# Kernel optimization log

Measured on AMD Instinct MI355X. Metric: run time of the kernel, lower is better.

## Reference

```python
import jax, jax.numpy as jnp
import numpy as np

MUL = 32          # channel multiplicity
N_NODES = 50000
N_EDGES = 800000
IN_DIM = 4 * MUL      # 32x0e + 32x1o (ir_mul layout: 1o block is (3, MUL))
SH_DIM = 4            # 0e + 1o
W_DIM = 5 * MUL       # 5 CG paths, per-channel weights
OUT_DIM = 7 * MUL     # 32x0e + 32x1o + 32x1e
INV_SQRT3 = 0.5773502691896258
INV_SQRT2 = 0.7071067811865476


def setup_inputs() -> dict:
    key = jax.random.key(0)
    k1, k2, k3, k4 = jax.random.split(key, 4)
    node_features = jax.random.normal(k1, (N_NODES, IN_DIM), dtype=jnp.float32)
    edge_angular = jax.random.normal(k2, (N_EDGES, SH_DIM), dtype=jnp.float32)
    edge_index = jax.random.randint(k3, (N_EDGES, 2), 0, N_NODES, dtype=jnp.int64)
    tp_weights = jax.random.normal(k4, (N_EDGES, W_DIM), dtype=jnp.float32)
    return {"node_features": node_features, "edge_angular": edge_angular,
            "edge_index": edge_index, "tp_weights": tp_weights}


def reference(node_features, edge_angular, edge_index, tp_weights):
    n_nodes = node_features.shape[0]
    src = edge_index[:, 0]
    dst = edge_index[:, 1]

    # gather sender node features per edge
    h = node_features[src]                       # (E, 4*MUL)
    h0 = h[:, :MUL]                              # (E, MUL)       32x0e
    h1 = h[:, MUL:].reshape(-1, 3, MUL)          # (E, 3, MUL)    32x1o, ir_mul layout

    y0 = edge_angular[:, 0:1]                    # (E, 1)   0e
    y1 = edge_angular[:, 1:4]                    # (E, 3)   1o

    w = tp_weights.reshape(-1, 5, MUL)           # (E, 5, MUL) per-path per-channel

    # path 0: 0e (x) 0e -> 0e ; path 3: 1o (x) 1o -> 0e (dot / sqrt(3))
    dot = jnp.einsum('emc,em->ec', h1, y1)       # (E, MUL)
    out0e = w[:, 0] * h0 * y0 + w[:, 3] * (INV_SQRT3 * dot)

    # path 1: 0e (x) 1o -> 1o ; path 2: 1o (x) 0e -> 1o
    out1o = (w[:, 1][:, None, :] * h0[:, None, :] * y1[:, :, None]
             + w[:, 2][:, None, :] * h1 * y0[:, :, None])     # (E, 3, MUL)

    # path 4: 1o (x) 1o -> 1e (cross / sqrt(2))
    c0 = h1[:, 1] * y1[:, 2, None] - h1[:, 2] * y1[:, 1, None]
    c1 = h1[:, 2] * y1[:, 0, None] - h1[:, 0] * y1[:, 2, None]
    c2 = h1[:, 0] * y1[:, 1, None] - h1[:, 1] * y1[:, 0, None]
    cross = jnp.stack([c0, c1, c2], axis=1)                   # (E, 3, MUL)
    out1e = w[:, 4][:, None, :] * (INV_SQRT2 * cross)

    msg = jnp.concatenate([out0e,
                           out1o.reshape(-1, 3 * MUL),
                           out1e.reshape(-1, 3 * MUL)], axis=1)  # (E, 7*MUL)

    # scatter-add messages into receiver nodes (size_out = n_nodes)
    out = jax.ops.segment_sum(msg, dst, num_segments=n_nodes)    # (N, 7*MUL)
    return out
```

## Files before the change

kernel.cpp:

```cpp
#include <hip/hip_runtime.h>


#define IN_DIM 128
#define W_DIM 160
#define OUT_DIM 224

typedef float vf4 __attribute__((ext_vector_type(4)));

__device__ __forceinline__ float elem(const float4& v, int i) {
    return ((const float*)&v)[i];
}

__global__ void __launch_bounds__(256) hist_dst(
    const int2* __restrict__ eidx2, int* __restrict__ counts, int n_edges)
{
    int e = blockIdx.x * blockDim.x + threadIdx.x;
    if (e >= n_edges) return;
    atomicAdd(counts + eidx2[e].y, 1);
}

__global__ void __launch_bounds__(256) block_sums(
    const int* __restrict__ counts, int* __restrict__ bsums, int n)
{
    int idx = blockIdx.x * 256 + threadIdx.x;
    int x = (idx < n) ? counts[idx] : 0;
    #pragma unroll
    for (int off = 1; off < 64; off <<= 1) x += __shfl_xor(x, off);
    __shared__ int ws[4];
    if ((threadIdx.x & 63) == 0) ws[threadIdx.x >> 6] = x;
    __syncthreads();
    if (threadIdx.x == 0) bsums[blockIdx.x] = ws[0] + ws[1] + ws[2] + ws[3];
}

__global__ void __launch_bounds__(256) scan_block_sums(
    int* __restrict__ bsums, int* __restrict__ total_out, int nb)
{
    __shared__ int wsum[4];
    __shared__ int carry_s;
    int tid = threadIdx.x;
    int lane = tid & 63, wid = tid >> 6;
    if (tid == 0) carry_s = 0;
    __syncthreads();

    for (int base = 0; base < nb; base += 256) {
        int idx = base + tid;
        int x = (idx < nb) ? bsums[idx] : 0;
        int incl = x;
        #pragma unroll
        for (int off = 1; off < 64; off <<= 1) {
            int v = __shfl_up(incl, off);
            if (lane >= off) incl += v;
        }
        if (lane == 63) wsum[wid] = incl;
        __syncthreads();
        int wpre = 0;
        #pragma unroll
        for (int k = 0; k < 4; ++k) if (k < wid) wpre += wsum[k];
        int carry = carry_s;
        int excl = incl - x + wpre + carry;
        if (idx < nb) bsums[idx] = excl;
        __syncthreads();
        if (tid == 255) carry_s = carry + wpre + incl;
        __syncthreads();
    }
    if (tid == 0) *total_out = carry_s;
}

__global__ void __launch_bounds__(256) scan_final(
    int* __restrict__ counts, int* __restrict__ cursor,
    const int* __restrict__ bsums, int n)
{
    int idx = blockIdx.x * 256 + threadIdx.x;
    int x = (idx < n) ? counts[idx] : 0;
    int lane = threadIdx.x & 63, wid = threadIdx.x >> 6;
    int incl = x;
    #pragma unroll
    for (int off = 1; off < 64; off <<= 1) {
        int v = __shfl_up(incl, off);
        if (lane >= off) incl += v;
    }
    __shared__ int wsum[4];
    if (lane == 63) wsum[wid] = incl;
    __syncthreads();
    int wpre = 0;
    #pragma unroll
    for (int k = 0; k < 4; ++k) if (k < wid) wpre += wsum[k];
    int excl = incl - x + wpre + bsums[blockIdx.x];
    if (idx < n) {
        counts[idx] = excl;
        cursor[idx] = excl;
    }
}

__global__ void __launch_bounds__(256) scatter_edges(
    const int2* __restrict__ eidx2, int* __restrict__ cursor,
    int2* __restrict__ pairs, int n_edges)
{
    int e = blockIdx.x * blockDim.x + threadIdx.x;
    if (e >= n_edges) return;
    int2 sd = eidx2[e];
    int pos = atomicAdd(cursor + sd.y, 1);
    pairs[pos] = make_int2(e, sd.x);
}

__global__ void __launch_bounds__(256) gather_nodes(
    const float* __restrict__ nf,
    const float* __restrict__ ang,
    const float* __restrict__ w,
    const int*  __restrict__ offsets,
    const int2* __restrict__ pairs,
    float* __restrict__ out,
    int n_nodes)
{
    const float INV_SQRT3 = 0.5773502691896258f;
    const float INV_SQRT2 = 0.7071067811865476f;

    int gtid = blockIdx.x * blockDim.x + threadIdx.x;
    int node = gtid >> 6;
    if (node >= n_nodes) return;
    int lane = threadIdx.x & 63;
    int c    = lane & 31;
    int half = lane >> 5;

    int start = offsets[node];
    int end   = offsets[node + 1];

    float a0 = 0.f, a1 = 0.f, a2 = 0.f, a3 = 0.f, a4 = 0.f, a5 = 0.f, a6 = 0.f;

    auto body = [&](int2 p) {
        int e = p.x, s = p.y;
        vf4 y = __builtin_nontemporal_load((const vf4*)(ang + 4 * (size_t)e));
        const float* hp = nf + (size_t)s * IN_DIM + c;
        float h0 = hp[0];
        float ha = hp[32];
        float hb = hp[64];
        float hc = hp[96];
        const float* wp = w + (size_t)e * W_DIM + c;
        float w0 = __builtin_nontemporal_load(wp);
        float w1 = __builtin_nontemporal_load(wp + 32);
        float w2 = __builtin_nontemporal_load(wp + 64);
        float w3 = __builtin_nontemporal_load(wp + 96);
        float w4 = __builtin_nontemporal_load(wp + 128);

        float dot = ha * y[1] + hb * y[2] + hc * y[3];
        a0 += w0 * h0 * y[0] + w3 * (INV_SQRT3 * dot);
        a1 += w1 * h0 * y[1] + w2 * ha * y[0];
        a2 += w1 * h0 * y[2] + w2 * hb * y[0];
        a3 += w1 * h0 * y[3] + w2 * hc * y[0];
        float w4s = w4 * INV_SQRT2;
        a4 += w4s * (hb * y[3] - hc * y[2]);
        a5 += w4s * (hc * y[1] - ha * y[3]);
        a6 += w4s * (ha * y[2] - hb * y[1]);
    };

    int i = start + half;
    for (; i + 2 < end; i += 4) {
        int2 pa = pairs[i];
        int2 pb = pairs[i + 2];
        body(pa);
        body(pb);
    }
    if (i < end) body(pairs[i]);

    a0 += __shfl_xor(a0, 32);
    a1 += __shfl_xor(a1, 32);
    a2 += __shfl_xor(a2, 32);
    a3 += __shfl_xor(a3, 32);
    a4 += __shfl_xor(a4, 32);
    a5 += __shfl_xor(a5, 32);
    a6 += __shfl_xor(a6, 32);

    if (half == 0) {
        float* op = out + (size_t)node * OUT_DIM + c;
        __builtin_nontemporal_store(a0, op);
        __builtin_nontemporal_store(a1, op + 32);
        __builtin_nontemporal_store(a2, op + 64);
        __builtin_nontemporal_store(a3, op + 96);
        __builtin_nontemporal_store(a4, op + 128);
        __builtin_nontemporal_store(a5, op + 160);
        __builtin_nontemporal_store(a6, op + 192);
    }
}

__global__ void __launch_bounds__(256) conv_tp_edges_atomic(
    const float* __restrict__ nf,
    const float* __restrict__ ang,
    const int*   __restrict__ eidx,
    const float* __restrict__ w,
    float* __restrict__ out,
    int n_edges)
{
    const float INV_SQRT3 = 0.5773502691896258f;
    const float INV_SQRT2 = 0.7071067811865476f;

    int tid = blockIdx.x * blockDim.x + threadIdx.x;
    int e = tid >> 3;
    int t = tid & 7;
    if (e >= n_edges) return;

    int src = eidx[2 * e];
    int dst = eidx[2 * e + 1];
    float4 y = *(const float4*)(ang + 4 * (size_t)e);

    const float* hp = nf + (size_t)src * IN_DIM + 4 * t;
    float4 h0  = *(const float4*)(hp);
    float4 h1a = *(const float4*)(hp + 32);
    float4 h1b = *(const float4*)(hp + 64);
    float4 h1c = *(const float4*)(hp + 96);

    const float* wp = w + (size_t)e * W_DIM + 4 * t;
    float4 w0 = *(const float4*)(wp);
    float4 w1 = *(const float4*)(wp + 32);
    float4 w2 = *(const float4*)(wp + 64);
    float4 w3 = *(const float4*)(wp + 96);
    float4 w4 = *(const float4*)(wp + 128);

    float* op = out + (size_t)dst * OUT_DIM + 4 * t;

    #pragma unroll
    for (int i = 0; i < 4; ++i) {
        float h0c = elem(h0, i), ha = elem(h1a, i), hb = elem(h1b, i), hc = elem(h1c, i);
        float dot = ha * y.y + hb * y.z + hc * y.w;
        atomicAdd(op + i, elem(w0, i) * h0c * y.x + elem(w3, i) * (INV_SQRT3 * dot));
        float w1c = elem(w1, i), w2c = elem(w2, i);
        atomicAdd(op + 32 + i, w1c * h0c * y.y + w2c * ha * y.x);
        atomicAdd(op + 64 + i, w1c * h0c * y.z + w2c * hb * y.x);
        atomicAdd(op + 96 + i, w1c * h0c * y.w + w2c * hc * y.x);
        float w4c = elem(w4, i) * INV_SQRT2;
        atomicAdd(op + 128 + i, w4c * (hb * y.w - hc * y.z));
        atomicAdd(op + 160 + i, w4c * (hc * y.y - ha * y.w));
        atomicAdd(op + 192 + i, w4c * (ha * y.z - hb * y.y));
    }
}

extern "C" void kernel_launch(void* const* d_in, const int* in_sizes, int n_in,
                              void* d_out, int out_size, void* d_ws, size_t ws_size,
                              hipStream_t stream) {
    const float* nf   = (const float*)d_in[0];
    const float* ang  = (const float*)d_in[1];
    const int*   eidx = (const int*)d_in[2];
    const float* w    = (const float*)d_in[3];
    float* out = (float*)d_out;

    int n_edges = in_sizes[2] / 2;
    int n_nodes = out_size / OUT_DIM;
    int nb = (n_nodes + 255) / 256;

    size_t off_counts = 0;
    size_t off_cursor = off_counts + (size_t)(n_nodes + 1);
    size_t off_bsums  = off_cursor + (size_t)n_nodes;
    size_t off_pairs  = (off_bsums + (size_t)nb + 1) & ~(size_t)1;
    size_t ints_needed = off_pairs + 2 * (size_t)n_edges;
    size_t bytes_needed = ints_needed * sizeof(int);

    if (ws_size < bytes_needed) {
        hipMemsetAsync(d_out, 0, (size_t)out_size * sizeof(float), stream);
        int threads_total = n_edges * 8;
        int grid = (threads_total + 255) / 256;
        conv_tp_edges_atomic<<<grid, 256, 0, stream>>>(nf, ang, eidx, w, out, n_edges);
        return;
    }

    int* counts  = (int*)d_ws + off_counts;
    int* cursor  = (int*)d_ws + off_cursor;
    int* bsums   = (int*)d_ws + off_bsums;
    int2* pairs  = (int2*)((int*)d_ws + off_pairs);

    hipMemsetAsync(counts, 0, (size_t)(n_nodes + 1) * sizeof(int), stream);

    int grid_e = (n_edges + 255) / 256;
    hist_dst<<<grid_e, 256, 0, stream>>>((const int2*)eidx, counts, n_edges);
    block_sums<<<nb, 256, 0, stream>>>(counts, bsums, n_nodes);
    scan_block_sums<<<1, 256, 0, stream>>>(bsums, counts + n_nodes, nb);
    scan_final<<<nb, 256, 0, stream>>>(counts, cursor, bsums, n_nodes);
    scatter_edges<<<grid_e, 256, 0, stream>>>((const int2*)eidx, cursor, pairs, n_edges);

    int threads_total = n_nodes * 64;
    int grid_g = (threads_total + 255) / 256;
    gather_nodes<<<grid_g, 256, 0, stream>>>(nf, ang, w, counts, pairs, out, n_nodes);
}
```

Measured before the change: 806.8 us.

## Software-pipeline gather loop with contiguous halves and two edges per thread in CSR build

```diff
diff --git a/kernel.cpp b/kernel.cpp
--- a/kernel.cpp
+++ b/kernel.cpp
@@ -6,17 +6,25 @@
 #define OUT_DIM 224
 
 typedef float vf4 __attribute__((ext_vector_type(4)));
+typedef int   vi4 __attribute__((ext_vector_type(4), aligned(8)));
 
 __device__ __forceinline__ float elem(const float4& v, int i) {
     return ((const float*)&v)[i];
 }
 
 __global__ void __launch_bounds__(256) hist_dst(
-    const int2* __restrict__ eidx2, int* __restrict__ counts, int n_edges)
-{
-    int e = blockIdx.x * blockDim.x + threadIdx.x;
-    if (e >= n_edges) return;
-    atomicAdd(counts + eidx2[e].y, 1);
+    const int* __restrict__ eidx, int* __restrict__ counts, int n_edges)
+{
+    int t = blockIdx.x * blockDim.x + threadIdx.x;
+    int e0 = 2 * t;
+    if (e0 >= n_edges) return;
+    if (e0 + 1 < n_edges) {
+        int4 q = *(const int4*)(eidx + 4 * (size_t)t);
+        atomicAdd(counts + q.y, 1);
+        atomicAdd(counts + q.w, 1);
+    } else {
+        atomicAdd(counts + eidx[2 * e0 + 1], 1);
+    }
 }
 
 __global__ void __launch_bounds__(256) block_sums(
@@ -93,15 +101,31 @@
 }
 
 __global__ void __launch_bounds__(256) scatter_edges(
-    const int2* __restrict__ eidx2, int* __restrict__ cursor,
+    const int* __restrict__ eidx, int* __restrict__ cursor,
     int2* __restrict__ pairs, int n_edges)
 {
-    int e = blockIdx.x * blockDim.x + threadIdx.x;
-    if (e >= n_edges) return;
-    int2 sd = eidx2[e];
-    int pos = atomicAdd(cursor + sd.y, 1);
-    pairs[pos] = make_int2(e, sd.x);
-}
+    int t = blockIdx.x * blockDim.x + threadIdx.x;
+    int e0 = 2 * t;
+    if (e0 >= n_edges) return;
+    if (e0 + 1 < n_edges) {
+        int4 q = *(const int4*)(eidx + 4 * (size_t)t);
+        int pos0 = atomicAdd(cursor + q.y, 1);
+        pairs[pos0] = make_int2(e0, q.x);
+        int pos1 = atomicAdd(cursor + q.w, 1);
+        pairs[pos1] = make_int2(e0 + 1, q.z);
+    } else {
+        int src = eidx[2 * e0];
+        int dst = eidx[2 * e0 + 1];
+        int pos = atomicAdd(cursor + dst, 1);
+        pairs[pos] = make_int2(e0, src);
+    }
+}
+
+struct EdgeRegs {
+    vf4  y;
+    float h0, ha, hb, hc;
+    float w0, w1, w2, w3, w4;
+};
 
 __global__ void __launch_bounds__(256) gather_nodes(
     const float* __restrict__ nf,
@@ -124,43 +148,72 @@
 
     int start = offsets[node];
     int end   = offsets[node + 1];
-
-    float a0 = 0.f, a1 = 0.f, a2 = 0.f, a3 = 0.f, a4 = 0.f, a5 = 0.f, a6 = 0.f;
-
-    auto body = [&](int2 p) {
-        int e = p.x, s = p.y;
-        vf4 y = __builtin_nontemporal_load((const vf4*)(ang + 4 * (size_t)e));
+    int cnt   = end - start;
+    int mid   = start + ((cnt + 1) >> 1);
+    int lo    = half ? mid : start;
+    int hi    = half ? end : mid;
+
+    auto load_edge = [&](EdgeRegs& E, int e, int s) {
+        const float* wp = w + (size_t)e * W_DIM + c;
+        E.w0 = __builtin_nontemporal_load(wp);
+        E.w1 = __builtin_nontemporal_load(wp + 32);
+        E.w2 = __builtin_nontemporal_load(wp + 64);
+        E.w3 = __builtin_nontemporal_load(wp + 96);
+        E.w4 = __builtin_nontemporal_load(wp + 128);
+        E.y  = __builtin_nontemporal_load((const vf4*)(ang + 4 * (size_t)e));
         const float* hp = nf + (size_t)s * IN_DIM + c;
-        float h0 = hp[0];
-        float ha = hp[32];
-        float hb = hp[64];
-        float hc = hp[96];
-        const float* wp = w + (size_t)e * W_DIM + c;
-        float w0 = __builtin_nontemporal_load(wp);
-        float w1 = __builtin_nontemporal_load(wp + 32);
-        float w2 = __builtin_nontemporal_load(wp + 64);
-        float w3 = __builtin_nontemporal_load(wp + 96);
-        float w4 = __builtin_nontemporal_load(wp + 128);
-
-        float dot = ha * y[1] + hb * y[2] + hc * y[3];
-        a0 += w0 * h0 * y[0] + w3 * (INV_SQRT3 * dot);
-        a1 += w1 * h0 * y[1] + w2 * ha * y[0];
-        a2 += w1 * h0 * y[2] + w2 * hb * y[0];
-        a3 += w1 * h0 * y[3] + w2 * hc * y[0];
-        float w4s = w4 * INV_SQRT2;
-        a4 += w4s * (hb * y[3] - hc * y[2]);
-        a5 += w4s * (hc * y[1] - ha * y[3]);
-        a6 += w4s * (ha * y[2] - hb * y[1]);
+        E.h0 = hp[0];
+        E.ha = hp[32];
+        E.hb = hp[64];
+        E.hc = hp[96];
     };
 
-    int i = start + half;
-    for (; i + 2 < end; i += 4) {
-        int2 pa = pairs[i];
-        int2 pb = pairs[i + 2];
-        body(pa);
-        body(pb);
-    }
-    if (i < end) body(pairs[i]);
+    float aA0 = 0.f, aA1 = 0.f, aA2 = 0.f, aA3 = 0.f, aA4 = 0.f, aA5 = 0.f, aA6 = 0.f;
+    float aB0 = 0.f, aB1 = 0.f, aB2 = 0.f, aB3 = 0.f, aB4 = 0.f, aB5 = 0.f, aB6 = 0.f;
+
+    #define COMPUTE(E, s0, s1, s2, s3, s4, s5, s6)                           \
+        do {                                                                 \
+            float dot = E.ha * E.y[1] + E.hb * E.y[2] + E.hc * E.y[3];       \
+            s0 += E.w0 * E.h0 * E.y[0] + E.w3 * (INV_SQRT3 * dot);           \
+            s1 += E.w1 * E.h0 * E.y[1] + E.w2 * E.ha * E.y[0];               \
+            s2 += E.w1 * E.h0 * E.y[2] + E.w2 * E.hb * E.y[0];               \
+            s3 += E.w1 * E.h0 * E.y[3] + E.w2 * E.hc * E.y[0];               \
+            float w4s = E.w4 * INV_SQRT2;                                    \
+            s4 += w4s * (E.hb * E.y[3] - E.hc * E.y[2]);                     \
+            s5 += w4s * (E.hc * E.y[1] - E.ha * E.y[3]);                     \
+            s6 += w4s * (E.ha * E.y[2] - E.hb * E.y[1]);                     \
+        } while (0)
+
+    int i = lo;
+    if (i + 1 < hi) {
+        vi4 q = *(const vi4*)(pairs + i);
+        EdgeRegs E0, E1;
+        load_edge(E0, q.x, q.y);
+        load_edge(E1, q.z, q.w);
+        i += 2;
+        for (; i + 1 < hi; i += 2) {
+            vi4 qn = *(const vi4*)(pairs + i);
+            EdgeRegs N0, N1;
+            load_edge(N0, qn.x, qn.y);
+            load_edge(N1, qn.z, qn.w);
+            COMPUTE(E0, aA0, aA1, aA2, aA3, aA4, aA5, aA6);
+            COMPUTE(E1, aB0, aB1, aB2, aB3, aB4, aB5, aB6);
+            E0 = N0;
+            E1 = N1;
+        }
+        COMPUTE(E0, aA0, aA1, aA2, aA3, aA4, aA5, aA6);
+        COMPUTE(E1, aB0, aB1, aB2, aB3, aB4, aB5, aB6);
+    }
+    if (i < hi) {
+        int2 p = pairs[i];
+        EdgeRegs E;
+        load_edge(E, p.x, p.y);
+        COMPUTE(E, aA0, aA1, aA2, aA3, aA4, aA5, aA6);
+    }
+    #undef COMPUTE
+
+    float a0 = aA0 + aB0, a1 = aA1 + aB1, a2 = aA2 + aB2, a3 = aA3 + aB3;
+    float a4 = aA4 + aB4, a5 = aA5 + aB5, a6 = aA6 + aB6;
 
     a0 += __shfl_xor(a0, 32);
     a1 += __shfl_xor(a1, 32);
@@ -268,12 +321,13 @@
 
     hipMemsetAsync(counts, 0, (size_t)(n_nodes + 1) * sizeof(int), stream);
 
-    int grid_e = (n_edges + 255) / 256;
-    hist_dst<<<grid_e, 256, 0, stream>>>((const int2*)eidx, counts, n_edges);
+    int half_e = (n_edges + 1) / 2;
+    int grid_e2 = (half_e + 255) / 256;
+    hist_dst<<<grid_e2, 256, 0, stream>>>(eidx, counts, n_edges);
     block_sums<<<nb, 256, 0, stream>>>(counts, bsums, n_nodes);
     scan_block_sums<<<1, 256, 0, stream>>>(bsums, counts + n_nodes, nb);
     scan_final<<<nb, 256, 0, stream>>>(counts, cursor, bsums, n_nodes);
-    scatter_edges<<<grid_e, 256, 0, stream>>>((const int2*)eidx, cursor, pairs, n_edges);
+    scatter_edges<<<grid_e2, 256, 0, stream>>>(eidx, cursor, pairs, n_edges);
 
     int threads_total = n_nodes * 64;
     int grid_g = (threads_total + 255) / 256;
```

After: 796.6 us. No clear change (-1.3%).

## Replace CSR scan with fixed-capacity per-node buckets in one cooperative fused kernel

Applied to the files above, without the earlier changes.

```diff
diff --git a/kernel.cpp b/kernel.cpp
--- a/kernel.cpp
+++ b/kernel.cpp
@@ -1,198 +1,215 @@
 #include <hip/hip_runtime.h>
+#include <hip/hip_cooperative_groups.h>
+
+namespace cg = cooperative_groups;
 
 
 #define IN_DIM 128
 #define W_DIM 160
 #define OUT_DIM 224
+#define SPILL_CAP 4096
 
 typedef float vf4 __attribute__((ext_vector_type(4)));
+
+#define INV_SQRT3f 0.5773502691896258f
+#define INV_SQRT2f 0.7071067811865476f
+
+
+__device__ __forceinline__ void scatter_phase(
+    const int* __restrict__ eidx, int* __restrict__ cursor,
+    int* __restrict__ spill_cnt, int4* __restrict__ spill,
+    int2* __restrict__ buckets, int cap, int n_edges, int tid, int nthreads)
+{
+    int n_half = (n_edges + 1) >> 1;
+    for (int t = tid; t < n_half; t += nthreads) {
+        int e0 = 2 * t;
+        if (e0 + 1 < n_edges) {
+            int4 q = *(const int4*)(eidx + 4 * (size_t)t);
+            int p0 = atomicAdd(cursor + q.y, 1);
+            if (p0 < cap) buckets[(size_t)q.y * cap + p0] = make_int2(e0, q.x);
+            else { int sp = atomicAdd(spill_cnt, 1); if (sp < SPILL_CAP) spill[sp] = make_int4(e0, q.x, q.y, 0); }
+            int p1 = atomicAdd(cursor + q.w, 1);
+            if (p1 < cap) buckets[(size_t)q.w * cap + p1] = make_int2(e0 + 1, q.z);
+            else { int sp = atomicAdd(spill_cnt, 1); if (sp < SPILL_CAP) spill[sp] = make_int4(e0 + 1, q.z, q.w, 0); }
+        } else {
+            int src = eidx[2 * e0];
+            int dst = eidx[2 * e0 + 1];
+            int p = atomicAdd(cursor + dst, 1);
+            if (p < cap) buckets[(size_t)dst * cap + p] = make_int2(e0, src);
+            else { int sp = atomicAdd(spill_cnt, 1); if (sp < SPILL_CAP) spill[sp] = make_int4(e0, src, dst, 0); }
+        }
+    }
+}
+
+__device__ __forceinline__ void gather_phase(
+    const float* __restrict__ nf, const float* __restrict__ ang,
+    const float* __restrict__ w, const int* __restrict__ cursor,
+    const int2* __restrict__ buckets, int cap, float* __restrict__ out,
+    int n_nodes, int wave_id, int n_waves, int lane)
+{
+    int c    = lane & 31;
+    int half = lane >> 5;
+
+    for (int node = wave_id; node < n_nodes; node += n_waves) {
+        int cnt = cursor[node];
+        if (cnt > cap) cnt = cap;
+        const int2* bp = buckets + (size_t)node * cap;
+        int mid = (cnt + 1) >> 1;
+        int lo = half ? mid : 0;
+        int hi = half ? cnt : mid;
+
+        float a0 = 0.f, a1 = 0.f, a2 = 0.f, a3 = 0.f, a4 = 0.f, a5 = 0.f, a6 = 0.f;
+
+        for (int i = lo; i < hi; ++i) {
+            int2 p = bp[i];
+            int e = p.x, s = p.y;
+            vf4 y = __builtin_nontemporal_load((const vf4*)(ang + 4 * (size_t)e));
+            const float* hp = nf + (size_t)s * IN_DIM + c;
+            float h0 = hp[0];
+            float ha = hp[32];
+            float hb = hp[64];
+            float hc = hp[96];
+            const float* wp = w + (size_t)e * W_DIM + c;
+            float w0 = __builtin_nontemporal_load(wp);
+            float w1 = __builtin_nontemporal_load(wp + 32);
+            float w2 = __builtin_nontemporal_load(wp + 64);
+            float w3 = __builtin_nontemporal_load(wp + 96);
+            float w4 = __builtin_nontemporal_load(wp + 128);
+
+            float dot = ha * y[1] + hb * y[2] + hc * y[3];
+            a0 += w0 * h0 * y[0] + w3 * (INV_SQRT3f * dot);
+            a1 += w1 * h0 * y[1] + w2 * ha * y[0];
+            a2 += w1 * h0 * y[2] + w2 * hb * y[0];
+            a3 += w1 * h0 * y[3] + w2 * hc * y[0];
+            float w4s = w4 * INV_SQRT2f;
+            a4 += w4s * (hb * y[3] - hc * y[2]);
+            a5 += w4s * (hc * y[1] - ha * y[3]);
+            a6 += w4s * (ha * y[2] - hb * y[1]);
+        }
+
+        a0 += __shfl_xor(a0, 32);
+        a1 += __shfl_xor(a1, 32);
+        a2 += __shfl_xor(a2, 32);
+        a3 += __shfl_xor(a3, 32);
+        a4 += __shfl_xor(a4, 32);
+        a5 += __shfl_xor(a5, 32);
+        a6 += __shfl_xor(a6, 32);
+
+        if (half == 0) {
+            float* op = out + (size_t)node * OUT_DIM + c;
+            __builtin_nontemporal_store(a0, op);
+            __builtin_nontemporal_store(a1, op + 32);
+            __builtin_nontemporal_store(a2, op + 64);
+            __builtin_nontemporal_store(a3, op + 96);
+            __builtin_nontemporal_store(a4, op + 128);
+            __builtin_nontemporal_store(a5, op + 160);
+            __builtin_nontemporal_store(a6, op + 192);
+        }
+    }
+}
+
+__device__ __forceinline__ void spill_phase(
+    const float* __restrict__ nf, const float* __restrict__ ang,
+    const float* __restrict__ w, const int4* __restrict__ spill,
+    int n_spill, float* __restrict__ out, int tid, int nthreads)
+{
+    for (int i = tid; i < n_spill; i += nthreads) {
+        int4 s4 = spill[i];
+        int e = s4.x, s = s4.y, dst = s4.z;
+        vf4 y = *(const vf4*)(ang + 4 * (size_t)e);
+        for (int c = 0; c < 32; ++c) {
+            float h0 = nf[(size_t)s * IN_DIM + c];
+            float ha = nf[(size_t)s * IN_DIM + 32 + c];
+            float hb = nf[(size_t)s * IN_DIM + 64 + c];
+            float hc = nf[(size_t)s * IN_DIM + 96 + c];
+            const float* wp = w + (size_t)e * W_DIM + c;
+            float w0 = wp[0], w1 = wp[32], w2 = wp[64], w3 = wp[96], w4 = wp[128];
+            float* op = out + (size_t)dst * OUT_DIM + c;
+            float dot = ha * y[1] + hb * y[2] + hc * y[3];
+            atomicAdd(op,       w0 * h0 * y[0] + w3 * (INV_SQRT3f * dot));
+            atomicAdd(op + 32,  w1 * h0 * y[1] + w2 * ha * y[0]);
+            atomicAdd(op + 64,  w1 * h0 * y[2] + w2 * hb * y[0]);
+            atomicAdd(op + 96,  w1 * h0 * y[3] + w2 * hc * y[0]);
+            float w4s = w4 * INV_SQRT2f;
+            atomicAdd(op + 128, w4s * (hb * y[3] - hc * y[2]));
+            atomicAdd(op + 160, w4s * (hc * y[1] - ha * y[3]));
+            atomicAdd(op + 192, w4s * (ha * y[2] - hb * y[1]));
+        }
+    }
+}
+
+
+__global__ void __launch_bounds__(256, 4) fused_conv(
+    const float* __restrict__ nf, const float* __restrict__ ang,
+    const int* __restrict__ eidx, const float* __restrict__ w,
+    int* __restrict__ cursor, int* __restrict__ spill_cnt,
+    int4* __restrict__ spill, int2* __restrict__ buckets,
+    float* __restrict__ out, int n_edges, int n_nodes, int cap)
+{
+    cg::grid_group grid = cg::this_grid();
+    int tid = blockIdx.x * blockDim.x + threadIdx.x;
+    int nthreads = gridDim.x * blockDim.x;
+
+    scatter_phase(eidx, cursor, spill_cnt, spill, buckets, cap, n_edges, tid, nthreads);
+
+    __threadfence();
+    grid.sync();
+
+    int lane = threadIdx.x & 63;
+    int wave_id = tid >> 6;
+    int n_waves = nthreads >> 6;
+    gather_phase(nf, ang, w, cursor, buckets, cap, out, n_nodes, wave_id, n_waves, lane);
+
+    __threadfence();
+    grid.sync();
+
+    int n_spill = *spill_cnt;
+    if (n_spill > SPILL_CAP) n_spill = SPILL_CAP;
+    spill_phase(nf, ang, w, spill, n_spill, out, tid, nthreads);
+}
+
+
+__global__ void __launch_bounds__(256) scatter_k(
+    const int* __restrict__ eidx, int* __restrict__ cursor,
+    int* __restrict__ spill_cnt, int4* __restrict__ spill,
+    int2* __restrict__ buckets, int cap, int n_edges)
+{
+    int tid = blockIdx.x * blockDim.x + threadIdx.x;
+    scatter_phase(eidx, cursor, spill_cnt, spill, buckets, cap, n_edges,
+                  tid, gridDim.x * blockDim.x);
+}
+
+__global__ void __launch_bounds__(256) gather_k(
+    const float* __restrict__ nf, const float* __restrict__ ang,
+    const float* __restrict__ w, const int* __restrict__ cursor,
+    const int2* __restrict__ buckets, int cap, float* __restrict__ out, int n_nodes)
+{
+    int tid = blockIdx.x * blockDim.x + threadIdx.x;
+    gather_phase(nf, ang, w, cursor, buckets, cap, out, n_nodes,
+                 tid >> 6, (gridDim.x * blockDim.x) >> 6, threadIdx.x & 63);
+}
+
+__global__ void __launch_bounds__(256) spill_k(
+    const float* __restrict__ nf, const float* __restrict__ ang,
+    const float* __restrict__ w, const int* __restrict__ spill_cnt,
+    const int4* __restrict__ spill, float* __restrict__ out)
+{
+    int n_spill = *spill_cnt;
+    if (n_spill > SPILL_CAP) n_spill = SPILL_CAP;
+    spill_phase(nf, ang, w, spill, n_spill, out,
+                blockIdx.x * blockDim.x + threadIdx.x, gridDim.x * blockDim.x);
+}
+
 
 __device__ __forceinline__ float elem(const float4& v, int i) {
     return ((const float*)&v)[i];
 }
 
-__global__ void __launch_bounds__(256) hist_dst(
-    const int2* __restrict__ eidx2, int* __restrict__ counts, int n_edges)
-{
-    int e = blockIdx.x * blockDim.x + threadIdx.x;
-    if (e >= n_edges) return;
-    atomicAdd(counts + eidx2[e].y, 1);
-}
-
-__global__ void __launch_bounds__(256) block_sums(
-    const int* __restrict__ counts, int* __restrict__ bsums, int n)
-{
-    int idx = blockIdx.x * 256 + threadIdx.x;
-    int x = (idx < n) ? counts[idx] : 0;
-    #pragma unroll
-    for (int off = 1; off < 64; off <<= 1) x += __shfl_xor(x, off);
-    __shared__ int ws[4];
-    if ((threadIdx.x & 63) == 0) ws[threadIdx.x >> 6] = x;
-    __syncthreads();
-    if (threadIdx.x == 0) bsums[blockIdx.x] = ws[0] + ws[1] + ws[2] + ws[3];
-}
-
-__global__ void __launch_bounds__(256) scan_block_sums(
-    int* __restrict__ bsums, int* __restrict__ total_out, int nb)
-{
-    __shared__ int wsum[4];
-    __shared__ int carry_s;
-    int tid = threadIdx.x;
-    int lane = tid & 63, wid = tid >> 6;
-    if (tid == 0) carry_s = 0;
-    __syncthreads();
-
-    for (int base = 0; base < nb; base += 256) {
-        int idx = base + tid;
-        int x = (idx < nb) ? bsums[idx] : 0;
-        int incl = x;
-        #pragma unroll
-        for (int off = 1; off < 64; off <<= 1) {
-            int v = __shfl_up(incl, off);
-            if (lane >= off) incl += v;
-        }
-        if (lane == 63) wsum[wid] = incl;
-        __syncthreads();
-        int wpre = 0;
-        #pragma unroll
-        for (int k = 0; k < 4; ++k) if (k < wid) wpre += wsum[k];
-        int carry = carry_s;
-        int excl = incl - x + wpre + carry;
-        if (idx < nb) bsums[idx] = excl;
-        __syncthreads();
-        if (tid == 255) carry_s = carry + wpre + incl;
-        __syncthreads();
-    }
-    if (tid == 0) *total_out = carry_s;
-}
-
-__global__ void __launch_bounds__(256) scan_final(
-    int* __restrict__ counts, int* __restrict__ cursor,
-    const int* __restrict__ bsums, int n)
-{
-    int idx = blockIdx.x * 256 + threadIdx.x;
-    int x = (idx < n) ? counts[idx] : 0;
-    int lane = threadIdx.x & 63, wid = threadIdx.x >> 6;
-    int incl = x;
-    #pragma unroll
-    for (int off = 1; off < 64; off <<= 1) {
-        int v = __shfl_up(incl, off);
-        if (lane >= off) incl += v;
-    }
-    __shared__ int wsum[4];
-    if (lane == 63) wsum[wid] = incl;
-    __syncthreads();
-    int wpre = 0;
-    #pragma unroll
-    for (int k = 0; k < 4; ++k) if (k < wid) wpre += wsum[k];
-    int excl = incl - x + wpre + bsums[blockIdx.x];
-    if (idx < n) {
-        counts[idx] = excl;
-        cursor[idx] = excl;
-    }
-}
-
-__global__ void __launch_bounds__(256) scatter_edges(
-    const int2* __restrict__ eidx2, int* __restrict__ cursor,
-    int2* __restrict__ pairs, int n_edges)
-{
-    int e = blockIdx.x * blockDim.x + threadIdx.x;
-    if (e >= n_edges) return;
-    int2 sd = eidx2[e];
-    int pos = atomicAdd(cursor + sd.y, 1);
-    pairs[pos] = make_int2(e, sd.x);
-}
-
-__global__ void __launch_bounds__(256) gather_nodes(
-    const float* __restrict__ nf,
-    const float* __restrict__ ang,
-    const float* __restrict__ w,
-    const int*  __restrict__ offsets,
-    const int2* __restrict__ pairs,
-    float* __restrict__ out,
-    int n_nodes)
-{
-    const float INV_SQRT3 = 0.5773502691896258f;
-    const float INV_SQRT2 = 0.7071067811865476f;
-
-    int gtid = blockIdx.x * blockDim.x + threadIdx.x;
-    int node = gtid >> 6;
-    if (node >= n_nodes) return;
-    int lane = threadIdx.x & 63;
-    int c    = lane & 31;
-    int half = lane >> 5;
-
-    int start = offsets[node];
-    int end   = offsets[node + 1];
-
-    float a0 = 0.f, a1 = 0.f, a2 = 0.f, a3 = 0.f, a4 = 0.f, a5 = 0.f, a6 = 0.f;
-
-    auto body = [&](int2 p) {
-        int e = p.x, s = p.y;
-        vf4 y = __builtin_nontemporal_load((const vf4*)(ang + 4 * (size_t)e));
-        const float* hp = nf + (size_t)s * IN_DIM + c;
-        float h0 = hp[0];
-        float ha = hp[32];
-        float hb = hp[64];
-        float hc = hp[96];
-        const float* wp = w + (size_t)e * W_DIM + c;
-        float w0 = __builtin_nontemporal_load(wp);
-        float w1 = __builtin_nontemporal_load(wp + 32);
-        float w2 = __builtin_nontemporal_load(wp + 64);
-        float w3 = __builtin_nontemporal_load(wp + 96);
-        float w4 = __builtin_nontemporal_load(wp + 128);
-
-        float dot = ha * y[1] + hb * y[2] + hc * y[3];
-        a0 += w0 * h0 * y[0] + w3 * (INV_SQRT3 * dot);
-        a1 += w1 * h0 * y[1] + w2 * ha * y[0];
-        a2 += w1 * h0 * y[2] + w2 * hb * y[0];
-        a3 += w1 * h0 * y[3] + w2 * hc * y[0];
-        float w4s = w4 * INV_SQRT2;
-        a4 += w4s * (hb * y[3] - hc * y[2]);
-        a5 += w4s * (hc * y[1] - ha * y[3]);
-        a6 += w4s * (ha * y[2] - hb * y[1]);
-    };
-
-    int i = start + half;
-    for (; i + 2 < end; i += 4) {
-        int2 pa = pairs[i];
-        int2 pb = pairs[i + 2];
-        body(pa);
-        body(pb);
-    }
-    if (i < end) body(pairs[i]);
-
-    a0 += __shfl_xor(a0, 32);
-    a1 += __shfl_xor(a1, 32);
-    a2 += __shfl_xor(a2, 32);
-    a3 += __shfl_xor(a3, 32);
-    a4 += __shfl_xor(a4, 32);
-    a5 += __shfl_xor(a5, 32);
-    a6 += __shfl_xor(a6, 32);
-
-    if (half == 0) {
-        float* op = out + (size_t)node * OUT_DIM + c;
-        __builtin_nontemporal_store(a0, op);
-        __builtin_nontemporal_store(a1, op + 32);
-        __builtin_nontemporal_store(a2, op + 64);
-        __builtin_nontemporal_store(a3, op + 96);
-        __builtin_nontemporal_store(a4, op + 128);
-        __builtin_nontemporal_store(a5, op + 160);
-        __builtin_nontemporal_store(a6, op + 192);
-    }
-}
-
 __global__ void __launch_bounds__(256) conv_tp_edges_atomic(
-    const float* __restrict__ nf,
-    const float* __restrict__ ang,
-    const int*   __restrict__ eidx,
-    const float* __restrict__ w,
-    float* __restrict__ out,
-    int n_edges)
-{
-    const float INV_SQRT3 = 0.5773502691896258f;
-    const float INV_SQRT2 = 0.7071067811865476f;
-
+    const float* __restrict__ nf, const float* __restrict__ ang,
+    const int* __restrict__ eidx, const float* __restrict__ w,
+    float* __restrict__ out, int n_edges)
+{
     int tid = blockIdx.x * blockDim.x + threadIdx.x;
     int e = tid >> 3;
     int t = tid & 7;
@@ -221,17 +238,18 @@
     for (int i = 0; i < 4; ++i) {
         float h0c = elem(h0, i), ha = elem(h1a, i), hb = elem(h1b, i), hc = elem(h1c, i);
         float dot = ha * y.y + hb * y.z + hc * y.w;
-        atomicAdd(op + i, elem(w0, i) * h0c * y.x + elem(w3, i) * (INV_SQRT3 * dot));
+        atomicAdd(op + i, elem(w0, i) * h0c * y.x + elem(w3, i) * (INV_SQRT3f * dot));
         float w1c = elem(w1, i), w2c = elem(w2, i);
         atomicAdd(op + 32 + i, w1c * h0c * y.y + w2c * ha * y.x);
         atomicAdd(op + 64 + i, w1c * h0c * y.z + w2c * hb * y.x);
         atomicAdd(op + 96 + i, w1c * h0c * y.w + w2c * hc * y.x);
-        float w4c = elem(w4, i) * INV_SQRT2;
+        float w4c = elem(w4, i) * INV_SQRT2f;
         atomicAdd(op + 128 + i, w4c * (hb * y.w - hc * y.z));
         atomicAdd(op + 160 + i, w4c * (hc * y.y - ha * y.w));
         atomicAdd(op + 192 + i, w4c * (ha * y.z - hb * y.y));
     }
 }
+
 
 extern "C" void kernel_launch(void* const* d_in, const int* in_sizes, int n_in,
                               void* d_out, int out_size, void* d_ws, size_t ws_size,
@@ -244,16 +262,18 @@
 
     int n_edges = in_sizes[2] / 2;
     int n_nodes = out_size / OUT_DIM;
-    int nb = (n_nodes + 255) / 256;
-
-    size_t off_counts = 0;
-    size_t off_cursor = off_counts + (size_t)(n_nodes + 1);
-    size_t off_bsums  = off_cursor + (size_t)n_nodes;
-    size_t off_pairs  = (off_bsums + (size_t)nb + 1) & ~(size_t)1;
-    size_t ints_needed = off_pairs + 2 * (size_t)n_edges;
-    size_t bytes_needed = ints_needed * sizeof(int);
-
-    if (ws_size < bytes_needed) {
+
+    size_t off_cursor = 0;
+    size_t off_spillc = off_cursor + (size_t)n_nodes;
+    size_t off_spill  = (off_spillc + 1 + 3) & ~(size_t)3;
+    size_t off_buckets = off_spill + 4 * (size_t)SPILL_CAP;
+
+    int cap = 2048;
+    while (cap >= 64 &&
+           (off_buckets + 2 * (size_t)n_nodes * (size_t)cap) * sizeof(int) > ws_size)
+        cap >>= 1;
+
+    if (cap < 64) {
         hipMemsetAsync(d_out, 0, (size_t)out_size * sizeof(float), stream);
         int threads_total = n_edges * 8;
         int grid = (threads_total + 255) / 256;
@@ -261,21 +281,35 @@
         return;
     }
 
-    int* counts  = (int*)d_ws + off_counts;
-    int* cursor  = (int*)d_ws + off_cursor;
-    int* bsums   = (int*)d_ws + off_bsums;
-    int2* pairs  = (int2*)((int*)d_ws + off_pairs);
-
-    hipMemsetAsync(counts, 0, (size_t)(n_nodes + 1) * sizeof(int), stream);
-
-    int grid_e = (n_edges + 255) / 256;
-    hist_dst<<<grid_e, 256, 0, stream>>>((const int2*)eidx, counts, n_edges);
-    block_sums<<<nb, 256, 0, stream>>>(counts, bsums, n_nodes);
-    scan_block_sums<<<1, 256, 0, stream>>>(bsums, counts + n_nodes, nb);
-    scan_final<<<nb, 256, 0, stream>>>(counts, cursor, bsums, n_nodes);
-    scatter_edges<<<grid_e, 256, 0, stream>>>((const int2*)eidx, cursor, pairs, n_edges);
-
-    int threads_total = n_nodes * 64;
-    int grid_g = (threads_total + 255) / 256;
-    gather_nodes<<<grid_g, 256, 0, stream>>>(nf, ang, w, counts, pairs, out, n_nodes);
-}
+    int*  cursor    = (int*)d_ws + off_cursor;
+    int*  spill_cnt = (int*)d_ws + off_spillc;
+    int4* spill     = (int4*)((int*)d_ws + off_spill);
+    int2* buckets   = (int2*)((int*)d_ws + off_buckets);
+
+    hipMemsetAsync(cursor, 0, ((size_t)n_nodes + 1) * sizeof(int), stream);
+
+    int maxb = 0;
+    hipError_t oe = hipOccupancyMaxActiveBlocksPerMultiprocessor(&maxb, fused_conv, 256, 0);
+    if (oe != hipSuccess || maxb < 1) maxb = 2;
+    if (maxb > 8) maxb = 8;
+    int grid = maxb * 256;
+
+    void* args[] = {
+        (void*)&nf, (void*)&ang, (void*)&eidx, (void*)&w,
+        (void*)&cursor, (void*)&spill_cnt, (void*)&spill, (void*)&buckets,
+        (void*)&out, (void*)&n_edges, (void*)&n_nodes, (void*)&cap
+    };
+    hipError_t le = hipLaunchCooperativeKernel((const void*)fused_conv,
+                                               dim3(grid), dim3(256),
+                                               args, 0, stream);
+    if (le != hipSuccess) {
+        int n_half = (n_edges + 1) / 2;
+        int grid_s = (n_half + 255) / 256;
+        scatter_k<<<grid_s, 256, 0, stream>>>(eidx, cursor, spill_cnt, spill,
+                                              buckets, cap, n_edges);
+        int grid_g = ((size_t)n_nodes * 64 + 255) / 256;
+        gather_k<<<grid_g, 256, 0, stream>>>(nf, ang, w, cursor, buckets, cap,
+                                             out, n_nodes);
+        spill_k<<<64, 256, 0, stream>>>(nf, ang, w, spill_cnt, spill, out);
+    }
+}
```

Result: slower. 1.305 ms (+61.8%).
